# Kernel optimization log

Measured on AMD Instinct MI355X. Metric: run time of the kernel, lower is better.

Reference implementation:

```python
import jax, jax.numpy as jnp
import numpy as np

GRID_H, GRID_W = 32, 32
THRESHOLD = 1.0
SMOOTH = 0.5


def setup_inputs() -> dict:
    key = jax.random.key(0)
    x = jax.random.normal(key, (64, GRID_H * GRID_W, 768), dtype=jnp.float32)
    return {"x": x}


def reference(x) -> jnp.ndarray:
    B, N, D = x.shape
    H, W = GRID_H, GRID_W
    xr = x.reshape(B, H, W, D)

    # L2 norm of neighbor differences (same as torch.norm(diff, dim=-1))
    diff_h = xr[:, :, 1:, :] - xr[:, :, :-1, :]            # [B, H, W-1, D]
    diff_v = xr[:, 1:, :, :] - xr[:, :-1, :, :]            # [B, H-1, W, D]
    anomaly_h = jnp.sqrt(jnp.sum(diff_h * diff_h, axis=-1))  # [B, H, W-1]
    anomaly_v = jnp.sqrt(jnp.sum(diff_v * diff_v, axis=-1))  # [B, H-1, W]

    # Torch code uses .any() over the batch dim: a patch is anomalous for ALL
    # batch elements if ANY batch element exceeds the threshold.
    exceed_h = jnp.any(anomaly_h > THRESHOLD, axis=0)      # [H, W-1]
    exceed_v = jnp.any(anomaly_v > THRESHOLD, axis=0)      # [H-1, W]

    # Interior patches: i in [1, H-2], j in [1, W-2].
    # Conditions checked per (i, j): ah[i, j-1], ah[i, j], av[i-1, j], av[i, j]
    mask = (exceed_h[1:H - 1, 0:W - 2]
            | exceed_h[1:H - 1, 1:W - 1]
            | exceed_v[0:H - 2, 1:W - 1]
            | exceed_v[1:H - 1, 1:W - 1])                  # [H-2, W-2]

    # 4-neighbor average (all reads from the ORIGINAL xr, as in the torch code)
    avg = (xr[:, 0:H - 2, 1:W - 1, :] + xr[:, 2:H, 1:W - 1, :]
           + xr[:, 1:H - 1, 0:W - 2, :] + xr[:, 1:H - 1, 2:W, :]) * 0.25

    center = xr[:, 1:H - 1, 1:W - 1, :]
    blended = (1.0 - SMOOTH) * center + SMOOTH * avg
    interior = jnp.where(mask[None, :, :, None], blended, center)

    out = xr.at[:, 1:H - 1, 1:W - 1, :].set(interior)
    return out.reshape(B, N, D)
```

## Files before the change

kernel.cpp:

```cpp
#include <hip/hip_runtime.h>

#define THRESH 1.0f

__global__ __launch_bounds__(256) void edge_flags_kernel(
    const float* __restrict__ x, int* __restrict__ flags) {
  __shared__ float red[4];
  __shared__ int sdone;
  const int e = blockIdx.x;
  const int t = threadIdx.x;
  if (t == 0) sdone = 0;
  __syncthreads();

  int p0, p1;
  if (e < 992) {
    int i = e / 31; int j = e - i * 31;
    p0 = i * 32 + j; p1 = p0 + 1;
  } else {
    int e2 = e - 992; int i = e2 >> 5; int j = e2 & 31;
    p0 = i * 32 + j; p1 = p0 + 32;
  }

  const int lane = t & 63;
  const int wid  = t >> 6;

  for (int b = 0; b < 64; ++b) {
    float s = 0.0f;
    if (t < 192) {
      const float4* A = (const float4*)(x + ((size_t)b * 1024 + p0) * 768);
      const float4* B = (const float4*)(x + ((size_t)b * 1024 + p1) * 768);
      float4 va = A[t];
      float4 vb = B[t];
      float dx = va.x - vb.x, dy = va.y - vb.y;
      float dz = va.z - vb.z, dw = va.w - vb.w;
      s = dx * dx + dy * dy + dz * dz + dw * dw;
    }
#pragma unroll
    for (int off = 32; off > 0; off >>= 1) s += __shfl_down(s, off, 64);
    if (lane == 0) red[wid] = s;
    __syncthreads();
    if (t == 0) {
      float tot = (red[0] + red[1]) + (red[2] + red[3]);
      if (tot > THRESH) sdone = 1;
    }
    __syncthreads();
    if (sdone) break;
  }
  if (t == 0) flags[e] = sdone;
}

__global__ void mask_kernel(const int* __restrict__ flags,
                            int* __restrict__ mask) {
  const int n = threadIdx.x;
  const int i = n >> 5, j = n & 31;
  int m = 0;
  if (i >= 1 && i <= 30 && j >= 1 && j <= 30) {
    const int* fh = flags;
    const int* fv = flags + 992;
    m = fh[i * 31 + (j - 1)] | fh[i * 31 + j] |
        fv[(i - 1) * 32 + j] | fv[i * 32 + j];
  }
  mask[n] = m;
}

__global__ __launch_bounds__(192) void apply_kernel(
    const float* __restrict__ x, const int* __restrict__ mask,
    float* __restrict__ out) {
  const int bn = blockIdx.x;
  const int n  = bn & 1023;
  const int t  = threadIdx.x;
  const size_t base = (size_t)bn * 192 + t;
  const float4* xv = (const float4*)x;
  float4* ov = (float4*)out;

  float4 c = xv[base];
  if (mask[n]) {
    float4 l = xv[base - 192];
    float4 r = xv[base + 192];
    float4 u = xv[base - 32 * 192];
    float4 d = xv[base + 32 * 192];
    float4 res;
    res.x = 0.5f * c.x + 0.125f * ((l.x + r.x) + (u.x + d.x));
    res.y = 0.5f * c.y + 0.125f * ((l.y + r.y) + (u.y + d.y));
    res.z = 0.5f * c.z + 0.125f * ((l.z + r.z) + (u.z + d.z));
    res.w = 0.5f * c.w + 0.125f * ((l.w + r.w) + (u.w + d.w));
    ov[base] = res;
  } else {
    ov[base] = c;
  }
}

extern "C" void kernel_launch(void* const* d_in, const int* in_sizes, int n_in,
                              void* d_out, int out_size, void* d_ws,
                              size_t ws_size, hipStream_t stream) {
  const float* x = (const float*)d_in[0];
  float* out = (float*)d_out;
  int* flags = (int*)d_ws;
  int* mask  = flags + 1984;

  edge_flags_kernel<<<1984, 256, 0, stream>>>(x, flags);
  mask_kernel<<<1, 1024, 0, stream>>>(flags, mask);
  apply_kernel<<<64 * 1024, 192, 0, stream>>>(x, mask, out);
}
```

Before: 344.3 us.

## Fuse edge-flag and mask computation per patch, remap apply blocks, nontemporal stores

Replaces the per-edge flag kernel and the single-block mask kernel with one per-patch kernel. Each block reads the centre and its four neighbours and checks all four edge norms together, exiting early once any batch exceeds the threshold. Border patches return at once. This drops one launch and the flags buffer, but each interior edge is now evaluated by two patches, so some reads are duplicated. The apply kernel also permutes its block index to interleave batches and writes output with nontemporal stores to avoid polluting the cache.

```diff
diff --git a/kernel.cpp b/kernel.cpp
--- a/kernel.cpp
+++ b/kernel.cpp
@@ -2,91 +2,91 @@
 
 #define THRESH 1.0f
 
-__global__ __launch_bounds__(256) void edge_flags_kernel(
-    const float* __restrict__ x, int* __restrict__ flags) {
-  __shared__ float red[4];
+typedef float nfloat4 __attribute__((ext_vector_type(4)));
+
+__device__ __forceinline__ float sqdiff4(float4 a, float4 b) {
+  float dx = a.x - b.x, dy = a.y - b.y, dz = a.z - b.z, dw = a.w - b.w;
+  return dx * dx + dy * dy + dz * dz + dw * dw;
+}
+
+__global__ __launch_bounds__(192) void mask_kernel(
+    const float* __restrict__ x, int* __restrict__ mask) {
+  const int n = blockIdx.x;
+  const int i = n >> 5, j = n & 31;
+  const int t = threadIdx.x;
+  if (i < 1 || i > 30 || j < 1 || j > 30) {
+    if (t == 0) mask[n] = 0;
+    return;
+  }
+  __shared__ float red[3][4];
   __shared__ int sdone;
-  const int e = blockIdx.x;
-  const int t = threadIdx.x;
   if (t == 0) sdone = 0;
   __syncthreads();
-
-  int p0, p1;
-  if (e < 992) {
-    int i = e / 31; int j = e - i * 31;
-    p0 = i * 32 + j; p1 = p0 + 1;
-  } else {
-    int e2 = e - 992; int i = e2 >> 5; int j = e2 & 31;
-    p0 = i * 32 + j; p1 = p0 + 32;
-  }
-
   const int lane = t & 63;
-  const int wid  = t >> 6;
+  const int wid = t >> 6;
+  const float4* xv = (const float4*)x;
 
   for (int b = 0; b < 64; ++b) {
-    float s = 0.0f;
-    if (t < 192) {
-      const float4* A = (const float4*)(x + ((size_t)b * 1024 + p0) * 768);
-      const float4* B = (const float4*)(x + ((size_t)b * 1024 + p1) * 768);
-      float4 va = A[t];
-      float4 vb = B[t];
-      float dx = va.x - vb.x, dy = va.y - vb.y;
-      float dz = va.z - vb.z, dw = va.w - vb.w;
-      s = dx * dx + dy * dy + dz * dz + dw * dw;
+    const size_t base = ((size_t)b * 1024 + n) * 192 + t;
+    float4 c = xv[base];
+    float4 l = xv[base - 192];
+    float4 r = xv[base + 192];
+    float4 u = xv[base - 32 * 192];
+    float4 d = xv[base + 32 * 192];
+    float sl = sqdiff4(c, l);
+    float sr = sqdiff4(r, c);
+    float su = sqdiff4(c, u);
+    float sd = sqdiff4(d, c);
+#pragma unroll
+    for (int off = 32; off > 0; off >>= 1) {
+      sl += __shfl_down(sl, off, 64);
+      sr += __shfl_down(sr, off, 64);
+      su += __shfl_down(su, off, 64);
+      sd += __shfl_down(sd, off, 64);
     }
-#pragma unroll
-    for (int off = 32; off > 0; off >>= 1) s += __shfl_down(s, off, 64);
-    if (lane == 0) red[wid] = s;
+    if (lane == 0) {
+      red[wid][0] = sl; red[wid][1] = sr;
+      red[wid][2] = su; red[wid][3] = sd;
+    }
     __syncthreads();
     if (t == 0) {
-      float tot = (red[0] + red[1]) + (red[2] + red[3]);
-      if (tot > THRESH) sdone = 1;
+      float L = red[0][0] + red[1][0] + red[2][0];
+      float R = red[0][1] + red[1][1] + red[2][1];
+      float U = red[0][2] + red[1][2] + red[2][2];
+      float D = red[0][3] + red[1][3] + red[2][3];
+      if (L > THRESH || R > THRESH || U > THRESH || D > THRESH) sdone = 1;
     }
     __syncthreads();
     if (sdone) break;
   }
-  if (t == 0) flags[e] = sdone;
-}
-
-__global__ void mask_kernel(const int* __restrict__ flags,
-                            int* __restrict__ mask) {
-  const int n = threadIdx.x;
-  const int i = n >> 5, j = n & 31;
-  int m = 0;
-  if (i >= 1 && i <= 30 && j >= 1 && j <= 30) {
-    const int* fh = flags;
-    const int* fv = flags + 992;
-    m = fh[i * 31 + (j - 1)] | fh[i * 31 + j] |
-        fv[(i - 1) * 32 + j] | fv[i * 32 + j];
-  }
-  mask[n] = m;
+  if (t == 0) mask[n] = sdone;
 }
 
 __global__ __launch_bounds__(192) void apply_kernel(
     const float* __restrict__ x, const int* __restrict__ mask,
     float* __restrict__ out) {
-  const int bn = blockIdx.x;
-  const int n  = bn & 1023;
-  const int t  = threadIdx.x;
+  const int orig = blockIdx.x;
+  const int bn = (orig & 7) * 8192 + (orig >> 3);
+  const int n = bn & 1023;
+  const int t = threadIdx.x;
   const size_t base = (size_t)bn * 192 + t;
   const float4* xv = (const float4*)x;
-  float4* ov = (float4*)out;
+  nfloat4* ov = (nfloat4*)out;
 
   float4 c = xv[base];
+  float4 res = c;
   if (mask[n]) {
     float4 l = xv[base - 192];
     float4 r = xv[base + 192];
     float4 u = xv[base - 32 * 192];
     float4 d = xv[base + 32 * 192];
-    float4 res;
     res.x = 0.5f * c.x + 0.125f * ((l.x + r.x) + (u.x + d.x));
     res.y = 0.5f * c.y + 0.125f * ((l.y + r.y) + (u.y + d.y));
     res.z = 0.5f * c.z + 0.125f * ((l.z + r.z) + (u.z + d.z));
     res.w = 0.5f * c.w + 0.125f * ((l.w + r.w) + (u.w + d.w));
-    ov[base] = res;
-  } else {
-    ov[base] = c;
   }
+  nfloat4 nres = {res.x, res.y, res.z, res.w};
+  __builtin_nontemporal_store(nres, ov + base);
 }
 
 extern "C" void kernel_launch(void* const* d_in, const int* in_sizes, int n_in,
@@ -94,10 +94,8 @@
                               size_t ws_size, hipStream_t stream) {
   const float* x = (const float*)d_in[0];
   float* out = (float*)d_out;
-  int* flags = (int*)d_ws;
-  int* mask  = flags + 1984;
+  int* mask = (int*)d_ws;
 
-  edge_flags_kernel<<<1984, 256, 0, stream>>>(x, flags);
-  mask_kernel<<<1, 1024, 0, stream>>>(flags, mask);
+  mask_kernel<<<1024, 192, 0, stream>>>(x, mask);
   apply_kernel<<<64 * 1024, 192, 0, stream>>>(x, mask, out);
 }
```

Result: no change. 348.2 us (+1.1%).
